# Performance work log

Hardware: AMD Instinct MI355X
Metric: run time of the kernel (lower is better)

The kernel has to match this reference:

```python
import jax, jax.numpy as jnp
import numpy as np

E4M3_MAX = 448.0
CHUNKS = 4  # module init: chunks=4, seg_mode='weight', equal chunksizes of out//chunks


def fp8_quant(v):
    # Simulate real e4m3 quantization: saturate then round-to-nearest e4m3, back to f32.
    return jnp.clip(v, -E4M3_MAX, E4M3_MAX).astype(jnp.float8_e4m3fn).astype(jnp.float32)


def setup_inputs() -> dict:
    key = jax.random.key(0)
    k1, k2, k3 = jax.random.split(key, 3)
    B, S, IN, OUT = 4, 4096, 4096, 4096
    x = jax.random.normal(k1, (B, S, IN), jnp.float32)
    w = jax.random.normal(k2, (OUT, IN), jnp.float32) * 0.02
    bias = jax.random.normal(k3, (OUT,), jnp.float32) * 0.01
    # Max-calibrated per-tensor scales (quantizer.scale from calibration)
    in_scale = jnp.max(jnp.abs(x)) / E4M3_MAX          # scalar
    wc = w.reshape(CHUNKS, OUT // CHUNKS, IN)
    w_scales = jnp.max(jnp.abs(wc), axis=(1, 2)) / E4M3_MAX  # [CHUNKS]
    return {"x": x, "w": w, "bias": bias, "in_scale": in_scale, "w_scales": w_scales}


def reference(x, w, bias, in_scale, w_scales):
    # seg_mode='weight': split weight along out_features into CHUNKS equal chunks,
    # run scaled e4m3 GEMM per chunk, concat outputs along out dim, add bias.
    OUT, IN = w.shape
    wc = w.reshape(CHUNKS, OUT // CHUNKS, IN)                 # [c, oc, i]
    xq = fp8_quant(x / in_scale)                              # [b, s, i]
    wq = fp8_quant(wc / w_scales[:, None, None])              # [c, oc, i]
    # out_i = (xq @ wq_i^T) * in_scale * w_scale_i  (dequant fused into GEMM epilogue)
    out = jnp.einsum('bsi,coi->bsco', xq, wq)
    out = out * (in_scale * w_scales)[None, None, :, None]
    out = out.reshape(x.shape[0], x.shape[1], OUT)            # concat chunk outputs
    return out + bias
```

## Files before the change

kernel.cpp:

```cpp
#include <hip/hip_runtime.h>
#include <stdint.h>

#define E4M3_MAX 448.0f

typedef float f32x4 __attribute__((ext_vector_type(4)));
typedef int   i32x4 __attribute__((ext_vector_type(4)));
typedef int   i32x8 __attribute__((ext_vector_type(8)));

__device__ __forceinline__ void gload_lds16(const void* g, void* l) {
    __builtin_amdgcn_global_load_lds(
        (__attribute__((address_space(1))) void*)(void*)g,
        (__attribute__((address_space(3))) void*)l,
        16, 0, 0);
}

__device__ __forceinline__ uint32_t quant4(float a, float b, float c, float d) {
    a = fminf(fmaxf(a, -E4M3_MAX), E4M3_MAX);
    b = fminf(fmaxf(b, -E4M3_MAX), E4M3_MAX);
    c = fminf(fmaxf(c, -E4M3_MAX), E4M3_MAX);
    d = fminf(fmaxf(d, -E4M3_MAX), E4M3_MAX);
    int q = 0;
    q = __builtin_amdgcn_cvt_pk_fp8_f32(a, b, q, false);
    q = __builtin_amdgcn_cvt_pk_fp8_f32(c, d, q, true);
    return (uint32_t)q;
}

__global__ void quant_x_kernel(const float* __restrict__ x,
                               const float* __restrict__ scale_p,
                               uint4* __restrict__ xq, int n16) {
    const float inv = 1.0f / scale_p[0];
    const int stride = gridDim.x * blockDim.x;
    for (int i = blockIdx.x * blockDim.x + threadIdx.x; i < n16; i += stride) {
        const float4* p = (const float4*)x + (size_t)i * 4;
        float4 v0 = p[0], v1 = p[1], v2 = p[2], v3 = p[3];
        uint4 q;
        q.x = quant4(v0.x * inv, v0.y * inv, v0.z * inv, v0.w * inv);
        q.y = quant4(v1.x * inv, v1.y * inv, v1.z * inv, v1.w * inv);
        q.z = quant4(v2.x * inv, v2.y * inv, v2.z * inv, v2.w * inv);
        q.w = quant4(v3.x * inv, v3.y * inv, v3.z * inv, v3.w * inv);
        xq[i] = q;
    }
}

__global__ void quant_w_kernel(const float* __restrict__ w,
                               const float* __restrict__ wsc,
                               uint4* __restrict__ wq, int n16, int chunk16) {
    const int stride = gridDim.x * blockDim.x;
    for (int i = blockIdx.x * blockDim.x + threadIdx.x; i < n16; i += stride) {
        const float inv = 1.0f / wsc[i / chunk16];
        const float4* p = (const float4*)w + (size_t)i * 4;
        float4 v0 = p[0], v1 = p[1], v2 = p[2], v3 = p[3];
        uint4 q;
        q.x = quant4(v0.x * inv, v0.y * inv, v0.z * inv, v0.w * inv);
        q.y = quant4(v1.x * inv, v1.y * inv, v1.z * inv, v1.w * inv);
        q.z = quant4(v2.x * inv, v2.y * inv, v2.z * inv, v2.w * inv);
        q.w = quant4(v3.x * inv, v3.y * inv, v3.z * inv, v3.w * inv);
        wq[i] = q;
    }
}

__device__ __forceinline__ i32x8 read_frag(const uint8_t* base, int o0, int o1) {
    i32x4 lo = *(const i32x4*)(base + o0);
    i32x4 hi = *(const i32x4*)(base + o1);
    return __builtin_shufflevector(lo, hi, 0, 1, 2, 3, 4, 5, 6, 7);
}

#define MFMA_MX(a, b, c) \
    __builtin_amdgcn_mfma_scale_f32_16x16x128_f8f6f4( \
        (a), (b), (c), 0, 0, 0, 0x7F7F7F7F, 0, 0x7F7F7F7F)

#define WAIT_LGKM(n)                                          \
    do {                                                      \
        asm volatile("s_waitcnt lgkmcnt(" #n ")" ::: "memory"); \
        __builtin_amdgcn_sched_barrier(0);                    \
    } while (0)

#define BM 256
#define BN 256
#define BKB 128

__global__ __launch_bounds__(512, 2) void gemm_fp8_kernel(
    const uint8_t* __restrict__ Aq, const uint8_t* __restrict__ Bq,
    const float* __restrict__ bias, const float* __restrict__ isp,
    const float* __restrict__ wsc, float* __restrict__ out,
    int M, int N, int K, int ocPerChunk) {
    __shared__ __align__(16) uint8_t lds[2][2][BM * BKB];

    const int tid  = threadIdx.x;
    const int lane = tid & 63;
    const int wid  = tid >> 6;
    const int wm   = wid >> 2;
    const int wn   = wid & 3;

    const int nwg = gridDim.x;
    const int cpx = nwg >> 3;
    const int swz = (blockIdx.x & 7) * cpx + (blockIdx.x >> 3);
    const int nbx = N / BN;
    const int bx  = swz % nbx;
    const int by  = swz / nbx;
    const int m0  = by * BM;
    const int n0  = bx * BN;

    const int lr   = lane & 15;
    const int sw   = (lr & 7) << 4;
    const int off0 = ((lane >> 4) * 32) ^ sw;
    const int off1 = off0 ^ 16;

    f32x4 acc[8][4] = {};

    const int nkt = K / BKB;

    auto stage = [&](int b, int kt) {
#pragma unroll
        for (int i = 0; i < 8; ++i) {
            const int idx = i * 512 + tid;
            const int row = idx >> 3;
            const int col = ((idx & 7) * 16) ^ ((row & 7) << 4);
            const uint8_t* src = (i < 4)
                ? Aq + (size_t)(m0 + row) * K + kt + col
                : Bq + (size_t)(n0 + (row - 256)) * K + kt + col;
            gload_lds16(src, &lds[b][0][0] + idx * 16);
        }
    };

    stage(0, 0);
    asm volatile("s_waitcnt vmcnt(0)" ::: "memory");
    __builtin_amdgcn_s_barrier();

    for (int t = 0; t < nkt; ++t) {
        const int cur = t & 1;
        const uint8_t* pa = &lds[cur][0][0] + (wm * 128 + lr) * BKB;
        const uint8_t* pb = &lds[cur][1][0] + (wn * 64  + lr) * BKB;

        i32x8 bv[4];
#pragma unroll
        for (int ni = 0; ni < 4; ni++)
            bv[ni] = read_frag(pb + ni * 16 * BKB, off0, off1);
        i32x8 a0 = read_frag(pa,            off0, off1);
        i32x8 a1 = read_frag(pa + 16 * BKB, off0, off1);
        i32x8 a2 = read_frag(pa + 32 * BKB, off0, off1);
        i32x8 a3 = read_frag(pa + 48 * BKB, off0, off1);
        if (t + 1 < nkt) stage(cur ^ 1, (t + 1) * BKB);

        WAIT_LGKM(4);
        __builtin_amdgcn_s_setprio(1);
#pragma unroll
        for (int ni = 0; ni < 4; ni++) {
            acc[0][ni] = MFMA_MX(a0, bv[ni], acc[0][ni]);
            acc[1][ni] = MFMA_MX(a1, bv[ni], acc[1][ni]);
        }
        __builtin_amdgcn_s_setprio(0);

        i32x8 a4 = read_frag(pa + 64 * BKB, off0, off1);
        i32x8 a5 = read_frag(pa + 80 * BKB, off0, off1);
        WAIT_LGKM(4);
        __builtin_amdgcn_s_setprio(1);
#pragma unroll
        for (int ni = 0; ni < 4; ni++) {
            acc[2][ni] = MFMA_MX(a2, bv[ni], acc[2][ni]);
            acc[3][ni] = MFMA_MX(a3, bv[ni], acc[3][ni]);
        }
        __builtin_amdgcn_s_setprio(0);

        i32x8 a6 = read_frag(pa + 96 * BKB,  off0, off1);
        i32x8 a7 = read_frag(pa + 112 * BKB, off0, off1);
        WAIT_LGKM(4);
        __builtin_amdgcn_s_setprio(1);
#pragma unroll
        for (int ni = 0; ni < 4; ni++) {
            acc[4][ni] = MFMA_MX(a4, bv[ni], acc[4][ni]);
            acc[5][ni] = MFMA_MX(a5, bv[ni], acc[5][ni]);
        }
        __builtin_amdgcn_s_setprio(0);

        WAIT_LGKM(0);
        __builtin_amdgcn_s_setprio(1);
#pragma unroll
        for (int ni = 0; ni < 4; ni++) {
            acc[6][ni] = MFMA_MX(a6, bv[ni], acc[6][ni]);
            acc[7][ni] = MFMA_MX(a7, bv[ni], acc[7][ni]);
        }
        __builtin_amdgcn_s_setprio(0);

        asm volatile("s_waitcnt vmcnt(0)" ::: "memory");
        __builtin_amdgcn_s_barrier();
    }

    const float is = isp[0];
#pragma unroll
    for (int ni = 0; ni < 4; ni++) {
        const int cidx = n0 + wn * 64 + ni * 16 + lr;
        const float sc = is * wsc[cidx / ocPerChunk];
        const float bs = bias[cidx];
#pragma unroll
        for (int mi = 0; mi < 8; mi++) {
            const int rbase = m0 + wm * 128 + mi * 16 + (lane >> 4) * 4;
#pragma unroll
            for (int j = 0; j < 4; j++)
                out[(size_t)(rbase + j) * N + cidx] = acc[mi][ni][j] * sc + bs;
        }
    }
}

extern "C" void kernel_launch(void* const* d_in, const int* in_sizes, int n_in,
                              void* d_out, int out_size, void* d_ws, size_t ws_size,
                              hipStream_t stream) {
    const float* x        = (const float*)d_in[0];
    const float* w        = (const float*)d_in[1];
    const float* bias     = (const float*)d_in[2];
    const float* in_scale = (const float*)d_in[3];
    const float* w_scales = (const float*)d_in[4];
    float* out = (float*)d_out;

    const int N = in_sizes[2];
    const int K = in_sizes[1] / N;
    const int M = in_sizes[0] / K;
    const int CHUNKS = in_sizes[4];
    const int ocPerChunk = N / CHUNKS;

    uint8_t* xq = (uint8_t*)d_ws;
    uint8_t* wq = xq + (size_t)M * K;

    const int xn16 = (int)(((size_t)M * K) / 16);
    const int wn16 = (int)(((size_t)N * K) / 16);
    const int chunk16 = (N / CHUNKS) * K / 16;

    quant_x_kernel<<<2048, 256, 0, stream>>>(x, in_scale, (uint4*)xq, xn16);
    quant_w_kernel<<<2048, 256, 0, stream>>>(w, w_scales, (uint4*)wq, wn16, chunk16);

    const int nblk = (M / BM) * (N / BN);
    gemm_fp8_kernel<<<dim3(nblk), 512, 0, stream>>>(xq, wq, bias, in_scale,
                                                    w_scales, out, M, N, K,
                                                    ocPerChunk);
}
```

Before: 372.8 us.

## Pre-shuffle quantized weights into MFMA fragment layout and load B directly to registers

The weight quantization kernel now writes fp8 weights in a fragment-major layout matching the MFMA B operand, so each lane can load its B fragment with two 16-byte global loads straight into registers. The B tile no longer goes through LDS, which halves LDS use and the async staging traffic. The block-to-tile mapping is also changed so each XCD works on a contiguous band of M rows. This trades LDS bandwidth and barriers for direct global or L2 reads of B in the inner loop, which add latency that the extra vmcnt waits must hide.

```diff
diff --git a/kernel.cpp b/kernel.cpp
--- a/kernel.cpp
+++ b/kernel.cpp
@@ -44,18 +44,35 @@
 
 __global__ void quant_w_kernel(const float* __restrict__ w,
                                const float* __restrict__ wsc,
-                               uint4* __restrict__ wq, int n16, int chunk16) {
+                               uint8_t* __restrict__ wq,
+                               int Nrows, int K, int chunkRows) {
+    const int nkt = K >> 7;
+    const int n32 = Nrows * (K >> 5);
     const int stride = gridDim.x * blockDim.x;
-    for (int i = blockIdx.x * blockDim.x + threadIdx.x; i < n16; i += stride) {
-        const float inv = 1.0f / wsc[i / chunk16];
-        const float4* p = (const float4*)w + (size_t)i * 4;
-        float4 v0 = p[0], v1 = p[1], v2 = p[2], v3 = p[3];
-        uint4 q;
-        q.x = quant4(v0.x * inv, v0.y * inv, v0.z * inv, v0.w * inv);
-        q.y = quant4(v1.x * inv, v1.y * inv, v1.z * inv, v1.w * inv);
-        q.z = quant4(v2.x * inv, v2.y * inv, v2.z * inv, v2.w * inv);
-        q.w = quant4(v3.x * inv, v3.y * inv, v3.z * inv, v3.w * inv);
-        wq[i] = q;
+    for (int i = blockIdx.x * blockDim.x + threadIdx.x; i < n32; i += stride) {
+        const int n  = i % Nrows;
+        const int k0 = (i / Nrows) << 5;
+        const float inv = 1.0f / wsc[n / chunkRows];
+        const float4* p = (const float4*)(w + (size_t)n * K + k0);
+        uint4 qa, qb;
+        {
+            float4 v0 = p[0], v1 = p[1], v2 = p[2], v3 = p[3];
+            qa.x = quant4(v0.x * inv, v0.y * inv, v0.z * inv, v0.w * inv);
+            qa.y = quant4(v1.x * inv, v1.y * inv, v1.z * inv, v1.w * inv);
+            qa.z = quant4(v2.x * inv, v2.y * inv, v2.z * inv, v2.w * inv);
+            qa.w = quant4(v3.x * inv, v3.y * inv, v3.z * inv, v3.w * inv);
+        }
+        {
+            float4 v0 = p[4], v1 = p[5], v2 = p[6], v3 = p[7];
+            qb.x = quant4(v0.x * inv, v0.y * inv, v0.z * inv, v0.w * inv);
+            qb.y = quant4(v1.x * inv, v1.y * inv, v1.z * inv, v1.w * inv);
+            qb.z = quant4(v2.x * inv, v2.y * inv, v2.z * inv, v2.w * inv);
+            qb.w = quant4(v3.x * inv, v3.y * inv, v3.z * inv, v3.w * inv);
+        }
+        const int kt = k0 >> 7, kg = (k0 >> 5) & 3, r = n & 15, nf = n >> 4;
+        uint8_t* dst = wq + (((size_t)nf * nkt + kt) * 64 + kg * 16 + r) * 32;
+        *(uint4*)dst = qa;
+        *(uint4*)(dst + 16) = qb;
     }
 }
 
@@ -69,10 +86,10 @@
     __builtin_amdgcn_mfma_scale_f32_16x16x128_f8f6f4( \
         (a), (b), (c), 0, 0, 0, 0x7F7F7F7F, 0, 0x7F7F7F7F)
 
-#define WAIT_LGKM(n)                                          \
-    do {                                                      \
+#define WAIT_LGKM(n)                                            \
+    do {                                                        \
         asm volatile("s_waitcnt lgkmcnt(" #n ")" ::: "memory"); \
-        __builtin_amdgcn_sched_barrier(0);                    \
+        __builtin_amdgcn_sched_barrier(0);                      \
     } while (0)
 
 #define BM 256
@@ -84,7 +101,7 @@
     const float* __restrict__ bias, const float* __restrict__ isp,
     const float* __restrict__ wsc, float* __restrict__ out,
     int M, int N, int K, int ocPerChunk) {
-    __shared__ __align__(16) uint8_t lds[2][2][BM * BKB];
+    __shared__ __align__(16) uint8_t As[2][BM * BKB];
 
     const int tid  = threadIdx.x;
     const int lane = tid & 63;
@@ -92,14 +109,15 @@
     const int wm   = wid >> 2;
     const int wn   = wid & 3;
 
-    const int nwg = gridDim.x;
-    const int cpx = nwg >> 3;
-    const int swz = (blockIdx.x & 7) * cpx + (blockIdx.x >> 3);
-    const int nbx = N / BN;
-    const int bx  = swz % nbx;
-    const int by  = swz / nbx;
-    const int m0  = by * BM;
-    const int n0  = bx * BN;
+    const int nbx   = N / BN;
+    const int nby   = M / BM;
+    const int chunk = nby >> 3;
+    const int xcd   = blockIdx.x & 7;
+    const int local = blockIdx.x >> 3;
+    const int bx    = local / chunk;
+    const int by    = xcd * chunk + (local % chunk);
+    const int m0    = by * BM;
+    const int n0    = bx * BN;
 
     const int lr   = lane & 15;
     const int sw   = (lr & 7) << 4;
@@ -110,16 +128,17 @@
 
     const int nkt = K / BKB;
 
+    const uint8_t* bbase =
+        Bq + ((size_t)((n0 >> 4) + wn * 4) * nkt) * 2048 + lane * 32;
+
     auto stage = [&](int b, int kt) {
 #pragma unroll
-        for (int i = 0; i < 8; ++i) {
+        for (int i = 0; i < 4; ++i) {
             const int idx = i * 512 + tid;
             const int row = idx >> 3;
             const int col = ((idx & 7) * 16) ^ ((row & 7) << 4);
-            const uint8_t* src = (i < 4)
-                ? Aq + (size_t)(m0 + row) * K + kt + col
-                : Bq + (size_t)(n0 + (row - 256)) * K + kt + col;
-            gload_lds16(src, &lds[b][0][0] + idx * 16);
+            gload_lds16(Aq + (size_t)(m0 + row) * K + kt + col,
+                        &As[b][0] + idx * 16);
         }
     };
 
@@ -129,19 +148,29 @@
 
     for (int t = 0; t < nkt; ++t) {
         const int cur = t & 1;
-        const uint8_t* pa = &lds[cur][0][0] + (wm * 128 + lr) * BKB;
-        const uint8_t* pb = &lds[cur][1][0] + (wn * 64  + lr) * BKB;
+        const uint8_t* pa = &As[cur][0] + (wm * 128 + lr) * BKB;
 
         i32x8 bv[4];
 #pragma unroll
-        for (int ni = 0; ni < 4; ni++)
-            bv[ni] = read_frag(pb + ni * 16 * BKB, off0, off1);
+        for (int ni = 0; ni < 4; ni++) {
+            const uint8_t* p = bbase + ((size_t)ni * nkt + t) * 2048;
+            i32x4 lo = *(const i32x4*)p;
+            i32x4 hi = *(const i32x4*)(p + 16);
+            bv[ni] = __builtin_shufflevector(lo, hi, 0, 1, 2, 3, 4, 5, 6, 7);
+        }
+        __builtin_amdgcn_sched_barrier(0);
+
         i32x8 a0 = read_frag(pa,            off0, off1);
         i32x8 a1 = read_frag(pa + 16 * BKB, off0, off1);
         i32x8 a2 = read_frag(pa + 32 * BKB, off0, off1);
         i32x8 a3 = read_frag(pa + 48 * BKB, off0, off1);
-        if (t + 1 < nkt) stage(cur ^ 1, (t + 1) * BKB);
-
+        __builtin_amdgcn_sched_barrier(0);
+        const bool pre = (t + 1 < nkt);
+        if (pre) stage(cur ^ 1, (t + 1) * BKB);
+        __builtin_amdgcn_sched_barrier(0);
+
+        if (pre) asm volatile("s_waitcnt vmcnt(4)" ::: "memory");
+        else     asm volatile("s_waitcnt vmcnt(0)" ::: "memory");
         WAIT_LGKM(4);
         __builtin_amdgcn_s_setprio(1);
 #pragma unroll
@@ -183,6 +212,7 @@
         __builtin_amdgcn_s_setprio(0);
 
         asm volatile("s_waitcnt vmcnt(0)" ::: "memory");
+        __builtin_amdgcn_sched_barrier(0);
         __builtin_amdgcn_s_barrier();
     }
 
@@ -222,11 +252,9 @@
     uint8_t* wq = xq + (size_t)M * K;
 
     const int xn16 = (int)(((size_t)M * K) / 16);
-    const int wn16 = (int)(((size_t)N * K) / 16);
-    const int chunk16 = (N / CHUNKS) * K / 16;
 
     quant_x_kernel<<<2048, 256, 0, stream>>>(x, in_scale, (uint4*)xq, xn16);
-    quant_w_kernel<<<2048, 256, 0, stream>>>(w, w_scales, (uint4*)wq, wn16, chunk16);
+    quant_w_kernel<<<2048, 256, 0, stream>>>(w, w_scales, wq, N, K, ocPerChunk);
 
     const int nblk = (M / BM) * (N / BN);
     gemm_fp8_kernel<<<dim3(nblk), 512, 0, stream>>>(xq, wq, bias, in_scale,
```

Result: slower. 422.2 us (+13.2%).

## Triple-buffer A tiles in LDS to prefetch two K-steps ahead

Applied to the files above, without the earlier changes.

Splits the shared LDS staging into separate A and B buffers, with A triple-buffered and B double-buffered. The A tile is now loaded two K iterations ahead and B one ahead, and the end-of-iteration wait is relaxed to vmcnt(4) so the newest A load can stay in flight across the barrier. The aim is to hide more global-to-LDS latency in the GEMM main loop. The cost is more LDS, 160KB in total, which leaves no headroom and rules out a second block per CU, plus extra buffer-index bookkeeping.

```diff
diff --git a/kernel.cpp b/kernel.cpp
--- a/kernel.cpp
+++ b/kernel.cpp
@@ -69,10 +69,10 @@
     __builtin_amdgcn_mfma_scale_f32_16x16x128_f8f6f4( \
         (a), (b), (c), 0, 0, 0, 0x7F7F7F7F, 0, 0x7F7F7F7F)
 
-#define WAIT_LGKM(n)                                          \
-    do {                                                      \
+#define WAIT_LGKM(n)                                            \
+    do {                                                        \
         asm volatile("s_waitcnt lgkmcnt(" #n ")" ::: "memory"); \
-        __builtin_amdgcn_sched_barrier(0);                    \
+        __builtin_amdgcn_sched_barrier(0);                      \
     } while (0)
 
 #define BM 256
@@ -84,7 +84,8 @@
     const float* __restrict__ bias, const float* __restrict__ isp,
     const float* __restrict__ wsc, float* __restrict__ out,
     int M, int N, int K, int ocPerChunk) {
-    __shared__ __align__(16) uint8_t lds[2][2][BM * BKB];
+    __shared__ __align__(16) uint8_t AsB[3][BM * BKB];
+    __shared__ __align__(16) uint8_t BsB[2][BN * BKB];
 
     const int tid  = threadIdx.x;
     const int lane = tid & 63;
@@ -110,27 +111,42 @@
 
     const int nkt = K / BKB;
 
-    auto stage = [&](int b, int kt) {
-#pragma unroll
-        for (int i = 0; i < 8; ++i) {
+    auto stage_A = [&](int b, int kt) {
+#pragma unroll
+        for (int i = 0; i < 4; ++i) {
             const int idx = i * 512 + tid;
             const int row = idx >> 3;
             const int col = ((idx & 7) * 16) ^ ((row & 7) << 4);
-            const uint8_t* src = (i < 4)
-                ? Aq + (size_t)(m0 + row) * K + kt + col
-                : Bq + (size_t)(n0 + (row - 256)) * K + kt + col;
-            gload_lds16(src, &lds[b][0][0] + idx * 16);
+            gload_lds16(Aq + (size_t)(m0 + row) * K + kt + col,
+                        &AsB[b][0] + idx * 16);
         }
     };
-
-    stage(0, 0);
-    asm volatile("s_waitcnt vmcnt(0)" ::: "memory");
+    auto stage_B = [&](int b, int kt) {
+#pragma unroll
+        for (int i = 0; i < 4; ++i) {
+            const int idx = i * 512 + tid;
+            const int row = idx >> 3;
+            const int col = ((idx & 7) * 16) ^ ((row & 7) << 4);
+            gload_lds16(Bq + (size_t)(n0 + row) * K + kt + col,
+                        &BsB[b][0] + idx * 16);
+        }
+    };
+
+    stage_B(0, 0);
+    stage_A(0, 0);
+    if (nkt > 1) {
+        stage_A(1, BKB);
+        asm volatile("s_waitcnt vmcnt(4)" ::: "memory");
+    } else {
+        asm volatile("s_waitcnt vmcnt(0)" ::: "memory");
+    }
+    __builtin_amdgcn_sched_barrier(0);
     __builtin_amdgcn_s_barrier();
 
+    int ar = 0;
     for (int t = 0; t < nkt; ++t) {
-        const int cur = t & 1;
-        const uint8_t* pa = &lds[cur][0][0] + (wm * 128 + lr) * BKB;
-        const uint8_t* pb = &lds[cur][1][0] + (wn * 64  + lr) * BKB;
+        const uint8_t* pa = &AsB[ar][0] + (wm * 128 + lr) * BKB;
+        const uint8_t* pb = &BsB[t & 1][0] + (wn * 64 + lr) * BKB;
 
         i32x8 bv[4];
 #pragma unroll
@@ -140,7 +156,8 @@
         i32x8 a1 = read_frag(pa + 16 * BKB, off0, off1);
         i32x8 a2 = read_frag(pa + 32 * BKB, off0, off1);
         i32x8 a3 = read_frag(pa + 48 * BKB, off0, off1);
-        if (t + 1 < nkt) stage(cur ^ 1, (t + 1) * BKB);
+        if (t + 1 < nkt) stage_B((t + 1) & 1, (t + 1) * BKB);
+        if (t + 2 < nkt) stage_A(ar >= 1 ? ar - 1 : ar + 2, (t + 2) * BKB);
 
         WAIT_LGKM(4);
         __builtin_amdgcn_s_setprio(1);
@@ -182,8 +199,15 @@
         }
         __builtin_amdgcn_s_setprio(0);
 
-        asm volatile("s_waitcnt vmcnt(0)" ::: "memory");
+        if (t + 2 < nkt) {
+            asm volatile("s_waitcnt vmcnt(4)" ::: "memory");
+        } else {
+            asm volatile("s_waitcnt vmcnt(0)" ::: "memory");
+        }
+        __builtin_amdgcn_sched_barrier(0);
         __builtin_amdgcn_s_barrier();
+
+        ar = (ar >= 2) ? 0 : ar + 1;
     }
 
     const float is = isp[0];
```

New measurement: 440.3 us. 1.18x slower.
